# Kernel optimization log

Measured on AMD Instinct MI355X. Metric: run time of the kernel, lower is better.

## Reference

```python
import jax, jax.numpy as jnp
import numpy as np

NUM_NODES = 100000
NUM_EDGES = 1_600_000
FEAT = 32


def setup_inputs() -> dict:
    key = jax.random.key(0)
    k1, k2 = jax.random.split(key)
    msg = jax.random.normal(k1, (NUM_EDGES, FEAT), dtype=jnp.float32)
    edge_index = jax.random.randint(k2, (2, NUM_EDGES), 0, NUM_NODES, dtype=jnp.int64)
    return {"msg": msg, "edge_index": edge_index, "num_nodes": NUM_NODES}


def reference(msg, edge_index, num_nodes):
    # Scatter-add edge messages into target nodes (edge_index[1]).
    target_nodes = edge_index[1]
    # segment_sum == zeros(num_nodes, feat).at[target].add(msg)
    out = jax.ops.segment_sum(msg, target_nodes, num_segments=num_nodes)
    return out
```

## Files before the change

kernel.cpp:

```cpp
#include <hip/hip_runtime.h>


#define FEAT 32
#define SCAN_BS 1024
#define PART_BS 256
#define UNROLL 8

__global__ void hist_kernel(const int* __restrict__ tgt, int* __restrict__ cnt, int E) {
    int e = blockIdx.x * blockDim.x + threadIdx.x;
    if (e < E) atomicAdd(&cnt[tgt[e]], 1);
}

__global__ void scan_block_kernel(const int* __restrict__ cnt, int* __restrict__ off,
                                  int* __restrict__ psum, int N) {
    __shared__ int s[SCAN_BS];
    int i = blockIdx.x * SCAN_BS + threadIdx.x;
    s[threadIdx.x] = (i < N) ? cnt[i] : 0;
    __syncthreads();
    for (int d = 1; d < SCAN_BS; d <<= 1) {
        int t = (threadIdx.x >= d) ? s[threadIdx.x - d] : 0;
        __syncthreads();
        s[threadIdx.x] += t;
        __syncthreads();
    }
    if (i < N) off[i + 1] = s[threadIdx.x];
    if (threadIdx.x == SCAN_BS - 1) psum[blockIdx.x] = s[SCAN_BS - 1];
}

__global__ void scan_partials_kernel(int* __restrict__ psum, int nb) {
    __shared__ int s[PART_BS];
    int run = 0;
    for (int base = 0; base < nb; base += PART_BS) {
        int i = base + threadIdx.x;
        int v = (i < nb) ? psum[i] : 0;
        s[threadIdx.x] = v;
        __syncthreads();
        for (int d = 1; d < PART_BS; d <<= 1) {
            int t = (threadIdx.x >= d) ? s[threadIdx.x - d] : 0;
            __syncthreads();
            s[threadIdx.x] += t;
            __syncthreads();
        }
        if (i < nb) psum[i] = run + s[threadIdx.x] - v;
        run += s[PART_BS - 1];
        __syncthreads();
    }
}

__global__ void finalize_offsets_kernel(int* __restrict__ off, int* __restrict__ cnt,
                                        const int* __restrict__ psum, int N) {
    int i = blockIdx.x * SCAN_BS + threadIdx.x;
    if (i == 0) off[0] = 0;
    if (i < N) {
        int end = off[i + 1] + psum[blockIdx.x];
        off[i + 1] = end;
        cnt[i] = end - cnt[i];
    }
}

__global__ void scatter_ids_kernel(const int* __restrict__ tgt, int* __restrict__ cur,
                                   int* __restrict__ eid, int E) {
    int e = blockIdx.x * blockDim.x + threadIdx.x;
    if (e < E) {
        int pos = atomicAdd(&cur[tgt[e]], 1);
        eid[pos] = e;
    }
}

__global__ void gather_sum_kernel(const float* __restrict__ msg, const int* __restrict__ off,
                                  const int* __restrict__ eid, float* __restrict__ out,
                                  int total) {
    int i = blockIdx.x * blockDim.x + threadIdx.x;
    if (i >= total) return;
    int n = i >> 5, f = i & 31;
    int start = off[n], end = off[n + 1];
    float acc[UNROLL];
#pragma unroll
    for (int u = 0; u < UNROLL; ++u) acc[u] = 0.f;
    for (int j = start; j < end; j += UNROLL) {
#pragma unroll
        for (int u = 0; u < UNROLL; ++u) {
            int jj = j + u;
            int e = eid[jj < end ? jj : end - 1];
            float m = msg[(size_t)e * FEAT + f];
            acc[u] += (jj < end) ? m : 0.f;
        }
    }
    float r = 0.f;
#pragma unroll
    for (int u = 0; u < UNROLL; ++u) r += acc[u];
    out[i] = r;
}

extern "C" void kernel_launch(void* const* d_in, const int* in_sizes, int n_in,
                              void* d_out, int out_size, void* d_ws, size_t ws_size,
                              hipStream_t stream) {
    const float* msg = (const float*)d_in[0];
    const int* edge_index = (const int*)d_in[1];
    int E = in_sizes[0] / FEAT;
    int N = out_size / FEAT;
    const int* tgt = edge_index + E;

    int nb = (N + SCAN_BS - 1) / SCAN_BS;
    int* cnt  = (int*)d_ws;
    int* off  = cnt + N;
    int* psum = off + N + 1;
    int* eid  = psum + nb;

    hipMemsetAsync(cnt, 0, (size_t)N * sizeof(int), stream);

    hist_kernel<<<(E + 255) / 256, 256, 0, stream>>>(tgt, cnt, E);
    scan_block_kernel<<<nb, SCAN_BS, 0, stream>>>(cnt, off, psum, N);
    scan_partials_kernel<<<1, PART_BS, 0, stream>>>(psum, nb);
    finalize_offsets_kernel<<<nb, SCAN_BS, 0, stream>>>(off, cnt, psum, N);
    scatter_ids_kernel<<<(E + 255) / 256, 256, 0, stream>>>(tgt, cnt, eid, E);
    gather_sum_kernel<<<(out_size + 255) / 256, 256, 0, stream>>>(
        msg, off, eid, (float*)d_out, out_size);
}
```

Measured before the change: 501.7 us.

## Replace per-node CSR sort with coarse bucket counting sort and LDS reduction

Replaces the per-node histogram, scan and edge-id scatter, which use global atomics over 100k nodes, with a bucketed counting sort. Each bucket covers 128 nodes, and per-chunk histograms and cursor offsets are kept in shared memory. Edges are packed as a local-node/edge-id word, and each bucket is reduced by one block using LDS float atomics into a 128x32 accumulator before being written to the output. This cuts global atomic traffic and scan size, in exchange for shared-memory atomic contention and a 24-bit edge-id limit.

Result: slower. 682.4 us (+36.0%).

```diff
diff --git a/kernel.cpp b/kernel.cpp
--- a/kernel.cpp
+++ b/kernel.cpp
@@ -1,21 +1,32 @@
 #include <hip/hip_runtime.h>
 
 
-#define FEAT 32
+#define FEAT    32
+#define NPB     128
+#define CHUNK   16384
 #define SCAN_BS 1024
 #define PART_BS 256
-#define UNROLL 8
+#define MAXB    1024
 
-__global__ void hist_kernel(const int* __restrict__ tgt, int* __restrict__ cnt, int E) {
-    int e = blockIdx.x * blockDim.x + threadIdx.x;
-    if (e < E) atomicAdd(&cnt[tgt[e]], 1);
+__global__ void bucket_hist_kernel(const int* __restrict__ tgt, int* __restrict__ hist,
+                                   int E, int nblk, int NB) {
+    __shared__ int h[MAXB];
+    for (int k = threadIdx.x; k < NB; k += blockDim.x) h[k] = 0;
+    __syncthreads();
+    int base = blockIdx.x * CHUNK;
+    int end = min(base + CHUNK, E);
+    for (int i = base + threadIdx.x; i < end; i += blockDim.x)
+        atomicAdd(&h[tgt[i] >> 7], 1);
+    __syncthreads();
+    for (int k = threadIdx.x; k < NB; k += blockDim.x)
+        hist[k * nblk + blockIdx.x] = h[k];
 }
 
-__global__ void scan_block_kernel(const int* __restrict__ cnt, int* __restrict__ off,
-                                  int* __restrict__ psum, int N) {
+__global__ void scan_block_kernel(const int* __restrict__ in, int* __restrict__ off,
+                                  int* __restrict__ psum, int M) {
     __shared__ int s[SCAN_BS];
     int i = blockIdx.x * SCAN_BS + threadIdx.x;
-    s[threadIdx.x] = (i < N) ? cnt[i] : 0;
+    s[threadIdx.x] = (i < M) ? in[i] : 0;
     __syncthreads();
     for (int d = 1; d < SCAN_BS; d <<= 1) {
         int t = (threadIdx.x >= d) ? s[threadIdx.x - d] : 0;
@@ -23,7 +34,7 @@
         s[threadIdx.x] += t;
         __syncthreads();
     }
-    if (i < N) off[i + 1] = s[threadIdx.x];
+    if (i < M) off[i + 1] = s[threadIdx.x];
     if (threadIdx.x == SCAN_BS - 1) psum[blockIdx.x] = s[SCAN_BS - 1];
 }
 
@@ -47,49 +58,57 @@
     }
 }
 
-__global__ void finalize_offsets_kernel(int* __restrict__ off, int* __restrict__ cnt,
-                                        const int* __restrict__ psum, int N) {
+__global__ void finalize_offsets_kernel(int* __restrict__ off, const int* __restrict__ psum,
+                                        int M) {
     int i = blockIdx.x * SCAN_BS + threadIdx.x;
     if (i == 0) off[0] = 0;
-    if (i < N) {
-        int end = off[i + 1] + psum[blockIdx.x];
-        off[i + 1] = end;
-        cnt[i] = end - cnt[i];
+    if (i < M) off[i + 1] += psum[blockIdx.x];
+}
+
+__global__ void scatter_pack_kernel(const int* __restrict__ tgt, const int* __restrict__ off,
+                                    int* __restrict__ packed, int E, int nblk, int NB) {
+    __shared__ int cur[MAXB];
+    for (int k = threadIdx.x; k < NB; k += blockDim.x)
+        cur[k] = off[k * nblk + blockIdx.x];
+    __syncthreads();
+    int base = blockIdx.x * CHUNK;
+    int end = min(base + CHUNK, E);
+    for (int i = base + threadIdx.x; i < end; i += blockDim.x) {
+        int t = tgt[i];
+        int pos = atomicAdd(&cur[t >> 7], 1);
+        packed[pos] = ((t & (NPB - 1)) << 24) | i;
     }
 }
 
-__global__ void scatter_ids_kernel(const int* __restrict__ tgt, int* __restrict__ cur,
-                                   int* __restrict__ eid, int E) {
-    int e = blockIdx.x * blockDim.x + threadIdx.x;
-    if (e < E) {
-        int pos = atomicAdd(&cur[tgt[e]], 1);
-        eid[pos] = e;
-    }
-}
-
-__global__ void gather_sum_kernel(const float* __restrict__ msg, const int* __restrict__ off,
-                                  const int* __restrict__ eid, float* __restrict__ out,
-                                  int total) {
-    int i = blockIdx.x * blockDim.x + threadIdx.x;
-    if (i >= total) return;
-    int n = i >> 5, f = i & 31;
-    int start = off[n], end = off[n + 1];
-    float acc[UNROLL];
+__global__ void bucket_reduce_kernel(const float* __restrict__ msg,
+                                     const int* __restrict__ packed,
+                                     const int* __restrict__ off,
+                                     float* __restrict__ out,
+                                     int E, int nblk, int NB, int N) {
+    __shared__ float acc[NPB * FEAT];
+    for (int i = threadIdx.x; i < NPB * FEAT; i += blockDim.x) acc[i] = 0.f;
+    __syncthreads();
+    int k = blockIdx.x;
+    int s0 = off[k * nblk];
+    int s1 = (k + 1 < NB) ? off[(k + 1) * nblk] : E;
+    int slot = threadIdx.x >> 5;
+    int f = threadIdx.x & 31;
+    for (int j = s0; j < s1; j += 32) {
 #pragma unroll
-    for (int u = 0; u < UNROLL; ++u) acc[u] = 0.f;
-    for (int j = start; j < end; j += UNROLL) {
-#pragma unroll
-        for (int u = 0; u < UNROLL; ++u) {
-            int jj = j + u;
-            int e = eid[jj < end ? jj : end - 1];
-            float m = msg[(size_t)e * FEAT + f];
-            acc[u] += (jj < end) ? m : 0.f;
+        for (int u = 0; u < 4; ++u) {
+            int jj = j + u * 8 + slot;
+            int p = packed[jj < s1 ? jj : s1 - 1];
+            float m = msg[(size_t)(p & 0xFFFFFF) * FEAT + f];
+            if (jj < s1) atomicAdd(&acc[(p >> 24) * FEAT + f], m);
         }
     }
-    float r = 0.f;
-#pragma unroll
-    for (int u = 0; u < UNROLL; ++u) r += acc[u];
-    out[i] = r;
+    __syncthreads();
+    int nodebase = k * NPB;
+    for (int i = threadIdx.x; i < NPB * FEAT; i += blockDim.x) {
+        int l = i >> 5;
+        if (nodebase + l < N)
+            out[(size_t)(nodebase + l) * FEAT + (i & 31)] = acc[i];
+    }
 }
 
 extern "C" void kernel_launch(void* const* d_in, const int* in_sizes, int n_in,
@@ -101,19 +120,21 @@
     int N = out_size / FEAT;
     const int* tgt = edge_index + E;
 
-    int nb = (N + SCAN_BS - 1) / SCAN_BS;
-    int* cnt  = (int*)d_ws;
-    int* off  = cnt + N;
-    int* psum = off + N + 1;
-    int* eid  = psum + nb;
+    int NB   = (N + NPB - 1) / NPB;
+    int nblk = (E + CHUNK - 1) / CHUNK;
+    int M    = NB * nblk;
+    int nb2  = (M + SCAN_BS - 1) / SCAN_BS;
 
-    hipMemsetAsync(cnt, 0, (size_t)N * sizeof(int), stream);
+    int* hist   = (int*)d_ws;
+    int* off    = hist + M;
+    int* psum   = off + M + 1;
+    int* packed = psum + nb2;
 
-    hist_kernel<<<(E + 255) / 256, 256, 0, stream>>>(tgt, cnt, E);
-    scan_block_kernel<<<nb, SCAN_BS, 0, stream>>>(cnt, off, psum, N);
-    scan_partials_kernel<<<1, PART_BS, 0, stream>>>(psum, nb);
-    finalize_offsets_kernel<<<nb, SCAN_BS, 0, stream>>>(off, cnt, psum, N);
-    scatter_ids_kernel<<<(E + 255) / 256, 256, 0, stream>>>(tgt, cnt, eid, E);
-    gather_sum_kernel<<<(out_size + 255) / 256, 256, 0, stream>>>(
-        msg, off, eid, (float*)d_out, out_size);
+    bucket_hist_kernel<<<nblk, 256, 0, stream>>>(tgt, hist, E, nblk, NB);
+    scan_block_kernel<<<nb2, SCAN_BS, 0, stream>>>(hist, off, psum, M);
+    scan_partials_kernel<<<1, PART_BS, 0, stream>>>(psum, nb2);
+    finalize_offsets_kernel<<<nb2, SCAN_BS, 0, stream>>>(off, psum, M);
+    scatter_pack_kernel<<<nblk, 256, 0, stream>>>(tgt, off, packed, E, nblk, NB);
+    bucket_reduce_kernel<<<NB, 256, 0, stream>>>(msg, packed, off, (float*)d_out,
+                                                 E, nblk, NB, N);
 }
```
